# Kernel tuning notes

Measured on AMD Instinct MI355X. Metric: run time of the kernel, lower is better.

Reference implementation:

```python
import jax, jax.numpy as jnp
import numpy as np

B, A, N = 4, 256, 64
NCB, NF, NSB, DIMS = 128, 128, 50, 3
CUTOFF = 5.0
LOG2 = 0.6931471805599453


def ssp(x):
    # shifted softplus: softplus(x) - ln(2)
    return jax.nn.softplus(x) - LOG2


def mlp2(x, W1, b1, W2, b2):
    # Dense(act=ssp) -> Dense(linear)
    return ssp(x @ W1 + b1) @ W2 + b2


def setup_inputs():
    key = jax.random.key(0)
    ks = jax.random.split(key, 32)

    def w(k, shape):
        return jax.random.normal(k, shape, jnp.float32) / np.sqrt(shape[0]).astype(np.float32)

    return {
        "xi": jax.random.normal(ks[0], (B, A, NCB), jnp.float32),
        "r_ij": jax.random.uniform(ks[1], (B, A, N), jnp.float32) * CUTOFF,
        "cos_ij": jax.random.normal(ks[2], (B, A, N, DIMS), jnp.float32),
        "f_ij": jax.random.normal(ks[3], (B, A, N, NSB), jnp.float32),
        "neighbor_mask": jnp.ones((B, A, N), jnp.float32),
        "filt_W1": w(ks[4], (NSB, NF)), "filt_b1": jnp.zeros((NF,), jnp.float32),
        "filt_W2": w(ks[5], (NF, NF)), "filt_b2": jnp.zeros((NF,), jnp.float32),
        "in2f_W": w(ks[6], (NCB, NF)),
        "f2out_W": w(ks[7], (NF, NF)), "f2out_b": jnp.zeros((NF,), jnp.float32),
        "atom_W1": w(ks[8], (NF, NF)), "atom_b1": jnp.zeros((NF,), jnp.float32),
        "atom_W2": w(ks[9], (NF, NCB)), "atom_b2": jnp.zeros((NCB,), jnp.float32),
        "pair_W1": w(ks[10], (NF, NF)), "pair_b1": jnp.zeros((NF,), jnp.float32),
        "pair_W2": w(ks[11], (NF, NCB)), "pair_b2": jnp.zeros((NCB,), jnp.float32),
        "env_W1": w(ks[12], (NF, NF)), "env_b1": jnp.zeros((NF,), jnp.float32),
        "env_W2": w(ks[13], (NF, NCB)), "env_b2": jnp.zeros((NCB,), jnp.float32),
        "neighbors": jax.random.randint(ks[14], (B, A, N), 0, A),
    }


def reference(xi, r_ij, cos_ij, f_ij, neighbor_mask,
              filt_W1, filt_b1, filt_W2, filt_b2, in2f_W, f2out_W, f2out_b,
              atom_W1, atom_b1, atom_W2, atom_b2,
              pair_W1, pair_b1, pair_W2, pair_b2,
              env_W1, env_b1, env_W2, env_b2, neighbors):
    bidx = jnp.arange(B)[:, None, None]
    # --- FTLayer: filter net on Gaussian-expanded distances, cosine cutoff ---
    Wf = ssp(f_ij @ filt_W1 + filt_b1) @ filt_W2 + filt_b2            # [B,A,N,NF]
    C = 0.5 * (jnp.cos(r_ij * (jnp.pi / CUTOFF)) + 1.0) * (r_ij < CUTOFF)
    Wf = Wf * C[..., None]
    yj = (xi @ in2f_W)[bidx, neighbors]                               # gather -> [B,A,N,NF]
    v = ssp((yj * Wf) @ f2out_W + f2out_b)                            # [B,A,N,NF]
    # --- atom-wise channel (masked neighbor sum) ---
    vi = jnp.sum(v * neighbor_mask[..., None], axis=2)                # [B,A,NF]
    vi = mlp2(vi, atom_W1, atom_b1, atom_W2, atom_b2)                 # [B,A,NCB]
    # --- pair tensor: outer product with cosine basis ---
    vij = mlp2(v, pair_W1, pair_b1, pair_W2, pair_b2)                 # [B,A,N,NCB]
    Vij = vij[..., None] * cos_ij[..., None, :]                       # [B,A,N,NCB,3]
    # --- environment tensor: masked agg then second-order neighbor gather ---
    vik = mlp2(v, env_W1, env_b1, env_W2, env_b2)                     # [B,A,N,NCB]
    Vik = jnp.sum(vik[..., None] * cos_ij[..., None, :]
                  * neighbor_mask[..., None, None], axis=2)           # [B,A,NCB,3]
    Vjl = Vik[bidx, neighbors]                                        # [B,A,N,NCB,3]
    V = Vij + Vik[:, :, None] + Vjl                                   # [B,A,N,NCB,3]
    return vi, V
```

## Files before the change

kernel.cpp:

```cpp
#include <hip/hip_runtime.h>
#include <hip/hip_bf16.h>
#include <math.h>

#define B 4
#define A 256
#define NN 64
#define NCB 128
#define NF 128
#define NSB 50
#define BA (B*A)
#define PAIRS (BA*NN)

typedef __bf16 bf;
typedef __attribute__((ext_vector_type(8))) __bf16 bfrag8;
typedef __attribute__((ext_vector_type(4))) float ffrag4;

__device__ __attribute__((aligned(16))) bf    g_yib[BA*NF];
__device__ __attribute__((aligned(16))) bf    g_vij[(size_t)PAIRS*NCB];
__device__ __attribute__((aligned(16))) float g_vik[BA*NCB*3];
__device__ __attribute__((aligned(16))) bf g_tf1[NF*64];
__device__ __attribute__((aligned(16))) bf g_tf2[NF*NF];
__device__ __attribute__((aligned(16))) bf g_tfo[NF*NF];
__device__ __attribute__((aligned(16))) bf g_tp1[NF*NF];
__device__ __attribute__((aligned(16))) bf g_tp2[NF*NF];
__device__ __attribute__((aligned(16))) bf g_te1[NF*NF];
__device__ __attribute__((aligned(16))) bf g_te2[NF*NF];

__device__ __forceinline__ float ssp(float x){
    float e = __expf(-fabsf(x));
    return fmaxf(x, 0.f) + __logf(1.f + e) - 0.6931471805599453f;
}

__global__ __launch_bounds__(256)
void k_wt(const float* __restrict__ f1, const float* __restrict__ f2,
          const float* __restrict__ fo, const float* __restrict__ p1,
          const float* __restrict__ p2, const float* __restrict__ e1,
          const float* __restrict__ e2){
    int s = blockIdx.x >> 3, part = blockIdx.x & 7;
    const float* src; bf* dst; int kb, realK;
    if (s == 0){ src = f1; dst = g_tf1; kb = 6; realK = NSB; }
    else {
        kb = 7; realK = 128;
        src = (s==1)?f2:(s==2)?fo:(s==3)?p1:(s==4)?p2:(s==5)?e1:e2;
        dst = (s==1)?g_tf2:(s==2)?g_tfo:(s==3)?g_tp1:(s==4)?g_tp2:(s==5)?g_te1:g_te2;
    }
    int total = NF << kb;
    int chunk = total >> 3;
    int end = (part + 1) * chunk;
    for (int e = part*chunk + threadIdx.x; e < end; e += 256){
        int n = e >> kb, k = e & ((1<<kb)-1);
        dst[e] = (k < realK) ? (bf)src[k*NF + n] : (bf)0.f;
    }
}

__global__ __launch_bounds__(NF)
void k_yi(const float* __restrict__ xi, const float* __restrict__ W){
    int row = blockIdx.x, f = threadIdx.x;
    __shared__ float x[NCB];
    x[f] = xi[row*NCB + f];
    __syncthreads();
    float s = 0.f;
    #pragma unroll 16
    for (int c = 0; c < NCB; c++) s += x[c]*W[c*NF + f];
    g_yib[row*NF + f] = (bf)s;
}

__device__ __forceinline__ void stage_w128(bf* __restrict__ sW, const bf* __restrict__ g,
                                           int half, int tid){
    #pragma unroll
    for (int i = 0; i < 4; i++){
        int r  = i*16 + (tid >> 4);
        int cp = (tid & 15)*8;
        *(bfrag8*)&sW[r*136 + cp] = *(const bfrag8*)&g[(half*64 + r)*128 + cp];
    }
}
__device__ __forceinline__ void stage_w64(bf* __restrict__ sW, const bf* __restrict__ g,
                                          int half, int tid){
    #pragma unroll
    for (int i = 0; i < 2; i++){
        int r  = i*32 + (tid >> 3);
        int cp = (tid & 7)*8;
        *(bfrag8*)&sW[r*72 + cp] = *(const bfrag8*)&g[(half*64 + r)*64 + cp];
    }
}
__device__ __forceinline__ void gemm4(const bf* __restrict__ sW, const bfrag8 afr[4],
                                      ffrag4 acc[4], int q, int c16){
    #pragma unroll
    for (int nt = 0; nt < 4; nt++){
        ffrag4 a = {0.f,0.f,0.f,0.f};
        #pragma unroll
        for (int kt = 0; kt < 4; kt++){
            bfrag8 bv = *(const bfrag8*)&sW[(nt*16 + c16)*136 + kt*32 + q*8];
            a = __builtin_amdgcn_mfma_f32_16x16x32_bf16(afr[kt], bv, a, 0, 0, 0);
        }
        acc[nt] = a;
    }
}
__device__ __forceinline__ void gemm2(const bf* __restrict__ sW, const bfrag8 afr[2],
                                      ffrag4 acc[4], int q, int c16){
    #pragma unroll
    for (int nt = 0; nt < 4; nt++){
        ffrag4 a = {0.f,0.f,0.f,0.f};
        #pragma unroll
        for (int kt = 0; kt < 2; kt++){
            bfrag8 bv = *(const bfrag8*)&sW[(nt*16 + c16)*72 + kt*32 + q*8];
            a = __builtin_amdgcn_mfma_f32_16x16x32_bf16(afr[kt], bv, a, 0, 0, 0);
        }
        acc[nt] = a;
    }
}

#define RDA4(DST) { _Pragma("unroll") for (int kt = 0; kt < 4; kt++) \
    DST[kt] = *(const bfrag8*)&sX[arow*136 + kt*32 + q*8]; }

#define EPI_SSP(BIASP, H) \
    { _Pragma("unroll") for (int nt = 0; nt < 4; nt++){ \
        int col = ((H)*4 + nt)*16 + c16; \
        float bias = BIASP[col]; \
        _Pragma("unroll") for (int rg = 0; rg < 4; rg++){ \
            int row = w*16 + q*4 + rg; \
            sX[row*136 + col] = (bf)ssp(acc[nt][rg] + bias); \
        } } }

#define EPI_LIN(BIASP, H) \
    { _Pragma("unroll") for (int nt = 0; nt < 4; nt++){ \
        int col = ((H)*4 + nt)*16 + c16; \
        float bias = BIASP[col]; \
        _Pragma("unroll") for (int rg = 0; rg < 4; rg++){ \
            int row = w*16 + q*4 + rg; \
            sX[row*136 + col] = (bf)(acc[nt][rg] + bias); \
        } } }

__global__ __launch_bounds__(256, 4)
void k_main(const float* __restrict__ r_ij, const float* __restrict__ cos_ij,
            const float* __restrict__ f_ij, const float* __restrict__ mask,
            const int* __restrict__ neighbors,
            const float* __restrict__ fb1, const float* __restrict__ fb2,
            const float* __restrict__ f2b,
            const float* __restrict__ aW1, const float* __restrict__ ab1,
            const float* __restrict__ aW2, const float* __restrict__ ab2,
            const float* __restrict__ pb1, const float* __restrict__ pb2,
            const float* __restrict__ eb1, const float* __restrict__ eb2,
            float* __restrict__ out_vi){
    const int tid  = threadIdx.x;
    const int ba   = blockIdx.x;
    const int b    = ba >> 8;
    const int w    = tid >> 6;
    const int lane = tid & 63;
    const int q    = lane >> 4;
    const int c16  = lane & 15;
    const int arow = w*16 + c16;

    __shared__ __attribute__((aligned(16))) bf sW[64*136];
    __shared__ __attribute__((aligned(16))) bf sX[64*136];
    __shared__ float sCosM[64*4];
    __shared__ float sCr[64];
    __shared__ int   sJb[64];

    #pragma unroll
    for (int i = 0; i < 16; i++){
        int row = w*16 + i;
        float v = (lane < NSB) ? f_ij[(ba*64 + row)*NSB + lane] : 0.f;
        sX[row*136 + lane] = (bf)v;
    }
    if (lane < 16){
        int row = w*16 + lane;
        int p = ba*64 + row;
        sCosM[row*4+0] = cos_ij[p*3+0];
        sCosM[row*4+1] = cos_ij[p*3+1];
        sCosM[row*4+2] = cos_ij[p*3+2];
        sCosM[row*4+3] = mask[p];
        float r = r_ij[p];
        sCr[row] = (r < 5.f) ? 0.5f*(__cosf(r*0.62831853071795864769f) + 1.f) : 0.f;
        int j = neighbors[p] & (A-1);
        sJb[row] = (b*A + j)*NF;
    }

    bfrag8 afr[4], afrV[4], afr2[2]; ffrag4 acc[4];

    #pragma unroll
    for (int kt = 0; kt < 2; kt++) afr2[kt] = *(const bfrag8*)&sX[arow*136 + kt*32 + q*8];
    #pragma unroll
    for (int half = 0; half < 2; half++){
        if (half) __syncthreads();
        stage_w64(sW, g_tf1, half, tid);
        __syncthreads();
        gemm2(sW, afr2, acc, q, c16);
        EPI_SSP(fb1, half);
    }
    RDA4(afr);
    __syncthreads();

    #pragma unroll
    for (int half = 0; half < 2; half++){
        if (half) __syncthreads();
        stage_w128(sW, g_tf2, half, tid);
        __syncthreads();
        gemm4(sW, afr, acc, q, c16);
        #pragma unroll
        for (int nt = 0; nt < 4; nt++){
            int col = (half*4 + nt)*16 + c16;
            float bias = fb2[col];
            #pragma unroll
            for (int rg = 0; rg < 4; rg++){
                int row = w*16 + q*4 + rg;
                float wf = (acc[nt][rg] + bias) * sCr[row];
                sX[row*136 + col] = (bf)((float)g_yib[sJb[row] + col] * wf);
            }
        }
    }
    RDA4(afr);
    __syncthreads();

    float vsAll[8];
    #pragma unroll
    for (int t = 0; t < 8; t++) vsAll[t] = 0.f;
    #pragma unroll
    for (int half = 0; half < 2; half++){
        if (half) __syncthreads();
        stage_w128(sW, g_tfo, half, tid);
        __syncthreads();
        gemm4(sW, afr, acc, q, c16);
        #pragma unroll
        for (int nt = 0; nt < 4; nt++){
            int col = (half*4 + nt)*16 + c16;
            float bias = f2b[col];
            #pragma unroll
            for (int rg = 0; rg < 4; rg++){
                int row = w*16 + q*4 + rg;
                float v = ssp(acc[nt][rg] + bias);
                sX[row*136 + col] = (bf)v;
                vsAll[half*4 + nt] += v * sCosM[row*4+3];
            }
        }
    }
    RDA4(afrV);
    __syncthreads();

    #pragma unroll
    for (int half = 0; half < 2; half++){
        if (half) __syncthreads();
        stage_w128(sW, g_tp1, half, tid);
        __syncthreads();
        gemm4(sW, afrV, acc, q, c16);
        EPI_SSP(pb1, half);
    }
    RDA4(afr);
    __syncthreads();

    #pragma unroll
    for (int half = 0; half < 2; half++){
        if (half) __syncthreads();
        stage_w128(sW, g_tp2, half, tid);
        __syncthreads();
        gemm4(sW, afr, acc, q, c16);
        EPI_LIN(pb2, half);
    }
    #pragma unroll
    for (int i = 0; i < 4; i++){
        int row = w*16 + i*4 + (lane >> 4);
        int cp  = c16*8;
        *(bfrag8*)&g_vij[((size_t)ba*64 + row)*128 + cp] = *(const bfrag8*)&sX[row*136 + cp];
    }
    __syncthreads();

    #pragma unroll
    for (int half = 0; half < 2; half++){
        if (half) __syncthreads();
        stage_w128(sW, g_te1, half, tid);
        __syncthreads();
        gemm4(sW, afrV, acc, q, c16);
        EPI_SSP(eb1, half);
    }
    RDA4(afr);
    __syncthreads();

    float vkAll[8][3];
    #pragma unroll
    for (int t = 0; t < 8; t++){ vkAll[t][0]=0.f; vkAll[t][1]=0.f; vkAll[t][2]=0.f; }
    #pragma unroll
    for (int half = 0; half < 2; half++){
        if (half) __syncthreads();
        stage_w128(sW, g_te2, half, tid);
        __syncthreads();
        gemm4(sW, afr, acc, q, c16);
        #pragma unroll
        for (int nt = 0; nt < 4; nt++){
            float bias = eb2[(half*4 + nt)*16 + c16];
            #pragma unroll
            for (int rg = 0; rg < 4; rg++){
                int row = w*16 + q*4 + rg;
                float vik = (acc[nt][rg] + bias) * sCosM[row*4+3];
                vkAll[half*4 + nt][0] += vik * sCosM[row*4+0];
                vkAll[half*4 + nt][1] += vik * sCosM[row*4+1];
                vkAll[half*4 + nt][2] += vik * sCosM[row*4+2];
            }
        }
    }

    __syncthreads();
    float* const sVs   = (float*)sX;
    float* const sVk   = (float*)((char*)sX + 2048);
    float* const sVsum = (float*)((char*)sX + 8192);
    float* const sHa   = (float*)((char*)sX + 8704);
    #pragma unroll
    for (int t = 0; t < 8; t++){
        float v = vsAll[t];
        v += __shfl_xor(v, 16);
        v += __shfl_xor(v, 32);
        if (q == 0) sVs[w*128 + t*16 + c16] = v;
    }
    #pragma unroll
    for (int t = 0; t < 8; t++){
        #pragma unroll
        for (int d = 0; d < 3; d++){
            float v = vkAll[t][d];
            v += __shfl_xor(v, 16);
            v += __shfl_xor(v, 32);
            if (q == 0) sVk[w*384 + (t*16 + c16)*3 + d] = v;
        }
    }
    __syncthreads();

    for (int e = tid; e < 384; e += 256)
        g_vik[ba*384 + e] = sVk[e] + sVk[384+e] + sVk[768+e] + sVk[1152+e];
    if (tid < 128)
        sVsum[tid] = sVs[tid] + sVs[128+tid] + sVs[256+tid] + sVs[384+tid];
    __syncthreads();
    if (tid < 128){
        float acc2 = ab1[tid];
        #pragma unroll 16
        for (int k = 0; k < 128; k++) acc2 += sVsum[k]*aW1[k*128 + tid];
        sHa[tid] = ssp(acc2);
    }
    __syncthreads();
    if (tid < 128){
        float acc2 = ab2[tid];
        #pragma unroll 16
        for (int k = 0; k < 128; k++) acc2 += sHa[k]*aW2[k*128 + tid];
        out_vi[ba*128 + tid] = acc2;
    }
}

__global__ __launch_bounds__(256)
void k_V(const float* __restrict__ cos_ij, const int* __restrict__ nbrs,
         float* __restrict__ outV){
    const int ba  = blockIdx.x;
    const int b   = ba >> 8;
    const int tid = threadIdx.x;
    __shared__ __attribute__((aligned(16))) bf sVij[64*128];
    __shared__ float sVa[384];
    __shared__ float sC[64*4];
    __shared__ int   sJ[64];
    #pragma unroll
    for (int i = 0; i < 4; i++){
        int e8 = tid + i*256;
        *(bfrag8*)&sVij[e8*8] = *(const bfrag8*)&g_vij[(size_t)ba*8192 + e8*8];
    }
    for (int e = tid; e < 384; e += 256) sVa[e] = g_vik[ba*384 + e];
    if (tid < 64){
        int p = ba*64 + tid;
        sJ[tid] = (b*A + (nbrs[p] & (A-1)))*384;
        sC[tid*4+0] = cos_ij[p*3+0];
        sC[tid*4+1] = cos_ij[p*3+1];
        sC[tid*4+2] = cos_ij[p*3+2];
    }
    __syncthreads();
    float* const oBase = outV + (size_t)ba*24576;
    #pragma unroll 4
    for (int it = 0; it < 24; it++){
        int idx = (it*256 + tid)*4;
        int pl  = idx / 384;
        int e0  = idx - pl*384;
        ffrag4 va = *(const ffrag4*)&sVa[e0];
        ffrag4 vj = *(const ffrag4*)(g_vik + sJ[pl] + e0);
        ffrag4 o;
        #pragma unroll
        for (int j2 = 0; j2 < 4; j2++){
            int e = e0 + j2;
            int c = e / 3;
            int d = e - c*3;
            float vv = (float)sVij[pl*128 + c];
            o[j2] = fmaf(vv, sC[pl*4+d], va[j2] + vj[j2]);
        }
        __builtin_nontemporal_store(o, (ffrag4*)(oBase + idx));
    }
}

extern "C" void kernel_launch(void* const* d_in, const int* in_sizes, int n_in,
                              void* d_out, int out_size, void* d_ws, size_t ws_size,
                              hipStream_t stream){
    const float* xi      = (const float*)d_in[0];
    const float* r_ij    = (const float*)d_in[1];
    const float* cos_ij  = (const float*)d_in[2];
    const float* f_ij    = (const float*)d_in[3];
    const float* nmask   = (const float*)d_in[4];
    const float* fW1     = (const float*)d_in[5];
    const float* fb1     = (const float*)d_in[6];
    const float* fW2     = (const float*)d_in[7];
    const float* fb2     = (const float*)d_in[8];
    const float* in2f_W  = (const float*)d_in[9];
    const float* f2W     = (const float*)d_in[10];
    const float* f2b     = (const float*)d_in[11];
    const float* aW1     = (const float*)d_in[12];
    const float* ab1     = (const float*)d_in[13];
    const float* aW2     = (const float*)d_in[14];
    const float* ab2     = (const float*)d_in[15];
    const float* pW1     = (const float*)d_in[16];
    const float* pb1     = (const float*)d_in[17];
    const float* pW2     = (const float*)d_in[18];
    const float* pb2     = (const float*)d_in[19];
    const float* eW1     = (const float*)d_in[20];
    const float* eb1     = (const float*)d_in[21];
    const float* eW2     = (const float*)d_in[22];
    const float* eb2     = (const float*)d_in[23];
    const int*  nbrs     = (const int*)d_in[24];

    float* out_vi = (float*)d_out;
    float* outV   = (float*)d_out + BA*NCB;

    k_wt<<<56, 256, 0, stream>>>(fW1, fW2, f2W, pW1, pW2, eW1, eW2);
    k_yi<<<BA, NF, 0, stream>>>(xi, in2f_W);

    k_main<<<BA, 256, 0, stream>>>(r_ij, cos_ij, f_ij, nmask, nbrs,
                                   fb1, fb2, f2b,
                                   aW1, ab1, aW2, ab2,
                                   pb1, pb2, eb1, eb2,
                                   out_vi);

    k_V<<<BA, 256, 0, stream>>>(cos_ij, nbrs, outV);
}
```

Before: 235.8 us.

## Fuse V assembly into main kernel via grid barrier, merge prep kernels

Merges the weight-transpose and yi projection kernels into one launch, and folds the k_V output kernel into the main kernel. Pair-MLP outputs stay in registers instead of round-tripping through a bf16 global buffer, and a software grid-wide atomic barrier waits until all g_vik entries are written before the neighbor gather. The cost is a spin barrier that needs all 1024 blocks co-resident, which risks deadlock if occupancy is lower than expected. The output stores are also now scalar, strided writes rather than 16-byte vectorised ones.

```diff
diff --git a/kernel.cpp b/kernel.cpp
--- a/kernel.cpp
+++ b/kernel.cpp
@@ -16,8 +16,8 @@
 typedef __attribute__((ext_vector_type(4))) float ffrag4;
 
 __device__ __attribute__((aligned(16))) bf    g_yib[BA*NF];
-__device__ __attribute__((aligned(16))) bf    g_vij[(size_t)PAIRS*NCB];
 __device__ __attribute__((aligned(16))) float g_vik[BA*NCB*3];
+__device__ int g_bar = 0;
 __device__ __attribute__((aligned(16))) bf g_tf1[NF*64];
 __device__ __attribute__((aligned(16))) bf g_tf2[NF*NF];
 __device__ __attribute__((aligned(16))) bf g_tfo[NF*NF];
@@ -32,37 +32,41 @@
 }
 
 __global__ __launch_bounds__(256)
-void k_wt(const float* __restrict__ f1, const float* __restrict__ f2,
-          const float* __restrict__ fo, const float* __restrict__ p1,
-          const float* __restrict__ p2, const float* __restrict__ e1,
-          const float* __restrict__ e2){
-    int s = blockIdx.x >> 3, part = blockIdx.x & 7;
-    const float* src; bf* dst; int kb, realK;
-    if (s == 0){ src = f1; dst = g_tf1; kb = 6; realK = NSB; }
-    else {
-        kb = 7; realK = 128;
-        src = (s==1)?f2:(s==2)?fo:(s==3)?p1:(s==4)?p2:(s==5)?e1:e2;
-        dst = (s==1)?g_tf2:(s==2)?g_tfo:(s==3)?g_tp1:(s==4)?g_tp2:(s==5)?g_te1:g_te2;
-    }
-    int total = NF << kb;
-    int chunk = total >> 3;
-    int end = (part + 1) * chunk;
-    for (int e = part*chunk + threadIdx.x; e < end; e += 256){
-        int n = e >> kb, k = e & ((1<<kb)-1);
-        dst[e] = (k < realK) ? (bf)src[k*NF + n] : (bf)0.f;
-    }
-}
-
-__global__ __launch_bounds__(NF)
-void k_yi(const float* __restrict__ xi, const float* __restrict__ W){
-    int row = blockIdx.x, f = threadIdx.x;
-    __shared__ float x[NCB];
-    x[f] = xi[row*NCB + f];
-    __syncthreads();
-    float s = 0.f;
-    #pragma unroll 16
-    for (int c = 0; c < NCB; c++) s += x[c]*W[c*NF + f];
-    g_yib[row*NF + f] = (bf)s;
+void k_pre(const float* __restrict__ f1, const float* __restrict__ f2,
+           const float* __restrict__ fo, const float* __restrict__ p1,
+           const float* __restrict__ p2, const float* __restrict__ e1,
+           const float* __restrict__ e2,
+           const float* __restrict__ xi, const float* __restrict__ W){
+    __shared__ float x[2][NCB];
+    int blk = blockIdx.x;
+    if (blk == 0 && threadIdx.x == 0)
+        __hip_atomic_store(&g_bar, 0, __ATOMIC_RELAXED, __HIP_MEMORY_SCOPE_AGENT);
+    if (blk < 56){
+        int s = blk >> 3, part = blk & 7;
+        const float* src; bf* dst; int kb, realK;
+        if (s == 0){ src = f1; dst = g_tf1; kb = 6; realK = NSB; }
+        else {
+            kb = 7; realK = 128;
+            src = (s==1)?f2:(s==2)?fo:(s==3)?p1:(s==4)?p2:(s==5)?e1:e2;
+            dst = (s==1)?g_tf2:(s==2)?g_tfo:(s==3)?g_tp1:(s==4)?g_tp2:(s==5)?g_te1:g_te2;
+        }
+        int total = NF << kb;
+        int chunk = total >> 3;
+        int end = (part + 1) * chunk;
+        for (int e = part*chunk + threadIdx.x; e < end; e += 256){
+            int n = e >> kb, k = e & ((1<<kb)-1);
+            dst[e] = (k < realK) ? (bf)src[k*NF + n] : (bf)0.f;
+        }
+    } else {
+        int r = threadIdx.x >> 7, f = threadIdx.x & 127;
+        int row = (blk - 56)*2 + r;
+        x[r][f] = xi[row*NCB + f];
+        __syncthreads();
+        float s = 0.f;
+        #pragma unroll 16
+        for (int c = 0; c < NCB; c++) s += x[r][c]*W[c*NF + f];
+        g_yib[row*NF + f] = (bf)s;
+    }
 }
 
 __device__ __forceinline__ void stage_w128(bf* __restrict__ sW, const bf* __restrict__ g,
@@ -122,26 +126,17 @@
             sX[row*136 + col] = (bf)ssp(acc[nt][rg] + bias); \
         } } }
 
-#define EPI_LIN(BIASP, H) \
-    { _Pragma("unroll") for (int nt = 0; nt < 4; nt++){ \
-        int col = ((H)*4 + nt)*16 + c16; \
-        float bias = BIASP[col]; \
-        _Pragma("unroll") for (int rg = 0; rg < 4; rg++){ \
-            int row = w*16 + q*4 + rg; \
-            sX[row*136 + col] = (bf)(acc[nt][rg] + bias); \
-        } } }
-
 __global__ __launch_bounds__(256, 4)
-void k_main(const float* __restrict__ r_ij, const float* __restrict__ cos_ij,
-            const float* __restrict__ f_ij, const float* __restrict__ mask,
-            const int* __restrict__ neighbors,
-            const float* __restrict__ fb1, const float* __restrict__ fb2,
-            const float* __restrict__ f2b,
-            const float* __restrict__ aW1, const float* __restrict__ ab1,
-            const float* __restrict__ aW2, const float* __restrict__ ab2,
-            const float* __restrict__ pb1, const float* __restrict__ pb2,
-            const float* __restrict__ eb1, const float* __restrict__ eb2,
-            float* __restrict__ out_vi){
+void k_fused(const float* __restrict__ r_ij, const float* __restrict__ cos_ij,
+             const float* __restrict__ f_ij, const float* __restrict__ mask,
+             const int* __restrict__ neighbors,
+             const float* __restrict__ fb1, const float* __restrict__ fb2,
+             const float* __restrict__ f2b,
+             const float* __restrict__ aW1, const float* __restrict__ ab1,
+             const float* __restrict__ aW2, const float* __restrict__ ab2,
+             const float* __restrict__ pb1, const float* __restrict__ pb2,
+             const float* __restrict__ eb1, const float* __restrict__ eb2,
+             float* __restrict__ out_vi, float* __restrict__ outV){
     const int tid  = threadIdx.x;
     const int ba   = blockIdx.x;
     const int b    = ba >> 8;
@@ -248,19 +243,20 @@
     RDA4(afr);
     __syncthreads();
 
+    float vijR[8][4];
     #pragma unroll
     for (int half = 0; half < 2; half++){
         if (half) __syncthreads();
         stage_w128(sW, g_tp2, half, tid);
         __syncthreads();
         gemm4(sW, afr, acc, q, c16);
-        EPI_LIN(pb2, half);
-    }
-    #pragma unroll
-    for (int i = 0; i < 4; i++){
-        int row = w*16 + i*4 + (lane >> 4);
-        int cp  = c16*8;
-        *(bfrag8*)&g_vij[((size_t)ba*64 + row)*128 + cp] = *(const bfrag8*)&sX[row*136 + cp];
+        #pragma unroll
+        for (int nt = 0; nt < 4; nt++){
+            float bias = pb2[(half*4 + nt)*16 + c16];
+            #pragma unroll
+            for (int rg = 0; rg < 4; rg++)
+                vijR[half*4 + nt][rg] = acc[nt][rg] + bias;
+        }
     }
     __syncthreads();
 
@@ -303,6 +299,7 @@
     float* const sVk   = (float*)((char*)sX + 2048);
     float* const sVsum = (float*)((char*)sX + 8192);
     float* const sHa   = (float*)((char*)sX + 8704);
+    float* const sVa   = (float*)((char*)sX + 12288);
     #pragma unroll
     for (int t = 0; t < 8; t++){
         float v = vsAll[t];
@@ -322,8 +319,11 @@
     }
     __syncthreads();
 
-    for (int e = tid; e < 384; e += 256)
-        g_vik[ba*384 + e] = sVk[e] + sVk[384+e] + sVk[768+e] + sVk[1152+e];
+    for (int e = tid; e < 384; e += 256){
+        float s = sVk[e] + sVk[384+e] + sVk[768+e] + sVk[1152+e];
+        g_vik[ba*384 + e] = s;
+        sVa[e] = s;
+    }
     if (tid < 128)
         sVsum[tid] = sVs[tid] + sVs[128+tid] + sVs[256+tid] + sVs[384+tid];
     __syncthreads();
@@ -340,50 +340,32 @@
         for (int k = 0; k < 128; k++) acc2 += sHa[k]*aW2[k*128 + tid];
         out_vi[ba*128 + tid] = acc2;
     }
-}
-
-__global__ __launch_bounds__(256)
-void k_V(const float* __restrict__ cos_ij, const int* __restrict__ nbrs,
-         float* __restrict__ outV){
-    const int ba  = blockIdx.x;
-    const int b   = ba >> 8;
-    const int tid = threadIdx.x;
-    __shared__ __attribute__((aligned(16))) bf sVij[64*128];
-    __shared__ float sVa[384];
-    __shared__ float sC[64*4];
-    __shared__ int   sJ[64];
-    #pragma unroll
-    for (int i = 0; i < 4; i++){
-        int e8 = tid + i*256;
-        *(bfrag8*)&sVij[e8*8] = *(const bfrag8*)&g_vij[(size_t)ba*8192 + e8*8];
-    }
-    for (int e = tid; e < 384; e += 256) sVa[e] = g_vik[ba*384 + e];
-    if (tid < 64){
-        int p = ba*64 + tid;
-        sJ[tid] = (b*A + (nbrs[p] & (A-1)))*384;
-        sC[tid*4+0] = cos_ij[p*3+0];
-        sC[tid*4+1] = cos_ij[p*3+1];
-        sC[tid*4+2] = cos_ij[p*3+2];
-    }
-    __syncthreads();
-    float* const oBase = outV + (size_t)ba*24576;
-    #pragma unroll 4
-    for (int it = 0; it < 24; it++){
-        int idx = (it*256 + tid)*4;
-        int pl  = idx / 384;
-        int e0  = idx - pl*384;
-        ffrag4 va = *(const ffrag4*)&sVa[e0];
-        ffrag4 vj = *(const ffrag4*)(g_vik + sJ[pl] + e0);
-        ffrag4 o;
-        #pragma unroll
-        for (int j2 = 0; j2 < 4; j2++){
-            int e = e0 + j2;
-            int c = e / 3;
-            int d = e - c*3;
-            float vv = (float)sVij[pl*128 + c];
-            o[j2] = fmaf(vv, sC[pl*4+d], va[j2] + vj[j2]);
-        }
-        __builtin_nontemporal_store(o, (ffrag4*)(oBase + idx));
+
+    __threadfence();
+    __syncthreads();
+    if (tid == 0){
+        __hip_atomic_fetch_add(&g_bar, 1, __ATOMIC_ACQ_REL, __HIP_MEMORY_SCOPE_AGENT);
+        while (__hip_atomic_load(&g_bar, __ATOMIC_ACQUIRE, __HIP_MEMORY_SCOPE_AGENT) < BA)
+            __builtin_amdgcn_s_sleep(8);
+    }
+    __syncthreads();
+
+    float* const oV = outV + (size_t)ba*24576;
+    #pragma unroll
+    for (int t = 0; t < 8; t++){
+        int col = t*16 + c16;
+        float a0 = sVa[col*3+0], a1 = sVa[col*3+1], a2 = sVa[col*3+2];
+        #pragma unroll
+        for (int rg = 0; rg < 4; rg++){
+            int row = w*16 + q*4 + rg;
+            float vv = vijR[t][rg];
+            const float* vj = g_vik + sJb[row]*3 + col*3;
+            float c0 = sCosM[row*4+0], c1 = sCosM[row*4+1], c2 = sCosM[row*4+2];
+            float* o = oV + row*384 + col*3;
+            __builtin_nontemporal_store(fmaf(vv, c0, a0 + vj[0]), o+0);
+            __builtin_nontemporal_store(fmaf(vv, c1, a1 + vj[1]), o+1);
+            __builtin_nontemporal_store(fmaf(vv, c2, a2 + vj[2]), o+2);
+        }
     }
 }
 
@@ -419,14 +401,11 @@
     float* out_vi = (float*)d_out;
     float* outV   = (float*)d_out + BA*NCB;
 
-    k_wt<<<56, 256, 0, stream>>>(fW1, fW2, f2W, pW1, pW2, eW1, eW2);
-    k_yi<<<BA, NF, 0, stream>>>(xi, in2f_W);
-
-    k_main<<<BA, 256, 0, stream>>>(r_ij, cos_ij, f_ij, nmask, nbrs,
-                                   fb1, fb2, f2b,
-                                   aW1, ab1, aW2, ab2,
-                                   pb1, pb2, eb1, eb2,
-                                   out_vi);
-
-    k_V<<<BA, 256, 0, stream>>>(cos_ij, nbrs, outV);
-}
+    k_pre<<<568, 256, 0, stream>>>(fW1, fW2, f2W, pW1, pW2, eW1, eW2, xi, in2f_W);
+
+    k_fused<<<BA, 256, 0, stream>>>(r_ij, cos_ij, f_ij, nmask, nbrs,
+                                    fb1, fb2, f2b,
+                                    aW1, ab1, aW2, ab2,
+                                    pb1, pb2, eb1, eb2,
+                                    out_vi, outV);
+}
```

Result: slower. 470.7 us (+99.6%).

## Process two atoms per block and double-buffer weight staging in k_main

Applied to the files above, without the earlier changes.

k_main now runs 512 threads per block covering two atoms (128 pair rows), so each staged weight tile is reused by twice as many rows. Weight halves are double-buffered in shared memory, and the next half or next layer's weights load while the current half's MFMA and epilogue run, which removes one barrier per stage. The costs are more shared memory per block (about 70KB), fewer blocks in the grid (512), and a launch bound of 512 threads with 4 blocks that puts heavy pressure on registers.

```diff
diff --git a/kernel.cpp b/kernel.cpp
--- a/kernel.cpp
+++ b/kernel.cpp
@@ -68,20 +68,17 @@
 __device__ __forceinline__ void stage_w128(bf* __restrict__ sW, const bf* __restrict__ g,
                                            int half, int tid){
     #pragma unroll
-    for (int i = 0; i < 4; i++){
-        int r  = i*16 + (tid >> 4);
+    for (int i = 0; i < 2; i++){
+        int r  = i*32 + (tid >> 4);
         int cp = (tid & 15)*8;
         *(bfrag8*)&sW[r*136 + cp] = *(const bfrag8*)&g[(half*64 + r)*128 + cp];
     }
 }
 __device__ __forceinline__ void stage_w64(bf* __restrict__ sW, const bf* __restrict__ g,
                                           int half, int tid){
-    #pragma unroll
-    for (int i = 0; i < 2; i++){
-        int r  = i*32 + (tid >> 3);
-        int cp = (tid & 7)*8;
-        *(bfrag8*)&sW[r*72 + cp] = *(const bfrag8*)&g[(half*64 + r)*64 + cp];
-    }
+    int r  = tid >> 3;
+    int cp = (tid & 7)*8;
+    *(bfrag8*)&sW[r*72 + cp] = *(const bfrag8*)&g[(half*64 + r)*64 + cp];
 }
 __device__ __forceinline__ void gemm4(const bf* __restrict__ sW, const bfrag8 afr[4],
                                       ffrag4 acc[4], int q, int c16){
@@ -131,7 +128,39 @@
             sX[row*136 + col] = (bf)(acc[nt][rg] + bias); \
         } } }
 
-__global__ __launch_bounds__(256, 4)
+#define EPI_S2(H) \
+    { _Pragma("unroll") for (int nt = 0; nt < 4; nt++){ \
+        int col = ((H)*4 + nt)*16 + c16; \
+        float bias = fb2[col]; \
+        _Pragma("unroll") for (int rg = 0; rg < 4; rg++){ \
+            int row = w*16 + q*4 + rg; \
+            float wf = (acc[nt][rg] + bias) * sCr[row]; \
+            sX[row*136 + col] = (bf)((float)g_yib[sJb[row] + col] * wf); \
+        } } }
+
+#define EPI_S3(H) \
+    { _Pragma("unroll") for (int nt = 0; nt < 4; nt++){ \
+        int col = ((H)*4 + nt)*16 + c16; \
+        float bias = f2b[col]; \
+        _Pragma("unroll") for (int rg = 0; rg < 4; rg++){ \
+            int row = w*16 + q*4 + rg; \
+            float v = ssp(acc[nt][rg] + bias); \
+            sX[row*136 + col] = (bf)v; \
+            vsAll[(H)*4 + nt] += v * sCosM[row*4+3]; \
+        } } }
+
+#define EPI_VIK(H) \
+    { _Pragma("unroll") for (int nt = 0; nt < 4; nt++){ \
+        float bias = eb2[((H)*4 + nt)*16 + c16]; \
+        _Pragma("unroll") for (int rg = 0; rg < 4; rg++){ \
+            int row = w*16 + q*4 + rg; \
+            float vik = (acc[nt][rg] + bias) * sCosM[row*4+3]; \
+            vkAll[(H)*4 + nt][0] += vik * sCosM[row*4+0]; \
+            vkAll[(H)*4 + nt][1] += vik * sCosM[row*4+1]; \
+            vkAll[(H)*4 + nt][2] += vik * sCosM[row*4+2]; \
+        } } }
+
+__global__ __launch_bounds__(512, 4)
 void k_main(const float* __restrict__ r_ij, const float* __restrict__ cos_ij,
             const float* __restrict__ f_ij, const float* __restrict__ mask,
             const int* __restrict__ neighbors,
@@ -143,29 +172,30 @@
             const float* __restrict__ eb1, const float* __restrict__ eb2,
             float* __restrict__ out_vi){
     const int tid  = threadIdx.x;
-    const int ba   = blockIdx.x;
-    const int b    = ba >> 8;
+    const int blk  = blockIdx.x;
     const int w    = tid >> 6;
     const int lane = tid & 63;
     const int q    = lane >> 4;
     const int c16  = lane & 15;
     const int arow = w*16 + c16;
 
-    __shared__ __attribute__((aligned(16))) bf sW[64*136];
-    __shared__ __attribute__((aligned(16))) bf sX[64*136];
-    __shared__ float sCosM[64*4];
-    __shared__ float sCr[64];
-    __shared__ int   sJb[64];
+    __shared__ __attribute__((aligned(16))) bf sWp[2][64*136];
+    __shared__ __attribute__((aligned(16))) bf sX[128*136];
+    __shared__ float sCosM[128*4];
+    __shared__ float sCr[128];
+    __shared__ int   sJb[128];
 
     #pragma unroll
     for (int i = 0; i < 16; i++){
         int row = w*16 + i;
-        float v = (lane < NSB) ? f_ij[(ba*64 + row)*NSB + lane] : 0.f;
+        float v = (lane < NSB) ? f_ij[((size_t)blk*128 + row)*NSB + lane] : 0.f;
         sX[row*136 + lane] = (bf)v;
     }
     if (lane < 16){
         int row = w*16 + lane;
-        int p = ba*64 + row;
+        int p = blk*128 + row;
+        int ba = blk*2 + (row >> 6);
+        int b  = ba >> 8;
         sCosM[row*4+0] = cos_ij[p*3+0];
         sCosM[row*4+1] = cos_ij[p*3+1];
         sCosM[row*4+2] = cos_ij[p*3+2];
@@ -177,132 +207,90 @@
     }
 
     bfrag8 afr[4], afrV[4], afr2[2]; ffrag4 acc[4];
+    float vsAll[8];
+    #pragma unroll
+    for (int t = 0; t < 8; t++) vsAll[t] = 0.f;
+    float vkAll[8][3];
+    #pragma unroll
+    for (int t = 0; t < 8; t++){ vkAll[t][0]=0.f; vkAll[t][1]=0.f; vkAll[t][2]=0.f; }
 
     #pragma unroll
     for (int kt = 0; kt < 2; kt++) afr2[kt] = *(const bfrag8*)&sX[arow*136 + kt*32 + q*8];
-    #pragma unroll
-    for (int half = 0; half < 2; half++){
-        if (half) __syncthreads();
-        stage_w64(sW, g_tf1, half, tid);
-        __syncthreads();
-        gemm2(sW, afr2, acc, q, c16);
-        EPI_SSP(fb1, half);
-    }
+
+    stage_w64(sWp[0], g_tf1, 0, tid);
+    __syncthreads();
+
+    stage_w64(sWp[1], g_tf1, 1, tid);
+    gemm2(sWp[0], afr2, acc, q, c16);
+    EPI_SSP(fb1, 0);
+    __syncthreads();
+    stage_w128(sWp[0], g_tf2, 0, tid);
+    gemm2(sWp[1], afr2, acc, q, c16);
+    EPI_SSP(fb1, 1);
     RDA4(afr);
     __syncthreads();
-
-    #pragma unroll
-    for (int half = 0; half < 2; half++){
-        if (half) __syncthreads();
-        stage_w128(sW, g_tf2, half, tid);
-        __syncthreads();
-        gemm4(sW, afr, acc, q, c16);
-        #pragma unroll
-        for (int nt = 0; nt < 4; nt++){
-            int col = (half*4 + nt)*16 + c16;
-            float bias = fb2[col];
-            #pragma unroll
-            for (int rg = 0; rg < 4; rg++){
-                int row = w*16 + q*4 + rg;
-                float wf = (acc[nt][rg] + bias) * sCr[row];
-                sX[row*136 + col] = (bf)((float)g_yib[sJb[row] + col] * wf);
-            }
-        }
-    }
+    stage_w128(sWp[1], g_tf2, 1, tid);
+    gemm4(sWp[0], afr, acc, q, c16);
+    EPI_S2(0);
+    __syncthreads();
+    stage_w128(sWp[0], g_tfo, 0, tid);
+    gemm4(sWp[1], afr, acc, q, c16);
+    EPI_S2(1);
     RDA4(afr);
     __syncthreads();
-
-    float vsAll[8];
-    #pragma unroll
-    for (int t = 0; t < 8; t++) vsAll[t] = 0.f;
-    #pragma unroll
-    for (int half = 0; half < 2; half++){
-        if (half) __syncthreads();
-        stage_w128(sW, g_tfo, half, tid);
-        __syncthreads();
-        gemm4(sW, afr, acc, q, c16);
-        #pragma unroll
-        for (int nt = 0; nt < 4; nt++){
-            int col = (half*4 + nt)*16 + c16;
-            float bias = f2b[col];
-            #pragma unroll
-            for (int rg = 0; rg < 4; rg++){
-                int row = w*16 + q*4 + rg;
-                float v = ssp(acc[nt][rg] + bias);
-                sX[row*136 + col] = (bf)v;
-                vsAll[half*4 + nt] += v * sCosM[row*4+3];
-            }
-        }
-    }
+    stage_w128(sWp[1], g_tfo, 1, tid);
+    gemm4(sWp[0], afr, acc, q, c16);
+    EPI_S3(0);
+    __syncthreads();
+    stage_w128(sWp[0], g_tp1, 0, tid);
+    gemm4(sWp[1], afr, acc, q, c16);
+    EPI_S3(1);
     RDA4(afrV);
     __syncthreads();
-
-    #pragma unroll
-    for (int half = 0; half < 2; half++){
-        if (half) __syncthreads();
-        stage_w128(sW, g_tp1, half, tid);
-        __syncthreads();
-        gemm4(sW, afrV, acc, q, c16);
-        EPI_SSP(pb1, half);
-    }
+    stage_w128(sWp[1], g_tp1, 1, tid);
+    gemm4(sWp[0], afrV, acc, q, c16);
+    EPI_SSP(pb1, 0);
+    __syncthreads();
+    stage_w128(sWp[0], g_tp2, 0, tid);
+    gemm4(sWp[1], afrV, acc, q, c16);
+    EPI_SSP(pb1, 1);
     RDA4(afr);
     __syncthreads();
-
-    #pragma unroll
-    for (int half = 0; half < 2; half++){
-        if (half) __syncthreads();
-        stage_w128(sW, g_tp2, half, tid);
-        __syncthreads();
-        gemm4(sW, afr, acc, q, c16);
-        EPI_LIN(pb2, half);
-    }
+    stage_w128(sWp[1], g_tp2, 1, tid);
+    gemm4(sWp[0], afr, acc, q, c16);
+    EPI_LIN(pb2, 0);
+    __syncthreads();
+    stage_w128(sWp[0], g_te1, 0, tid);
+    gemm4(sWp[1], afr, acc, q, c16);
+    EPI_LIN(pb2, 1);
     #pragma unroll
     for (int i = 0; i < 4; i++){
         int row = w*16 + i*4 + (lane >> 4);
         int cp  = c16*8;
-        *(bfrag8*)&g_vij[((size_t)ba*64 + row)*128 + cp] = *(const bfrag8*)&sX[row*136 + cp];
-    }
-    __syncthreads();
-
-    #pragma unroll
-    for (int half = 0; half < 2; half++){
-        if (half) __syncthreads();
-        stage_w128(sW, g_te1, half, tid);
-        __syncthreads();
-        gemm4(sW, afrV, acc, q, c16);
-        EPI_SSP(eb1, half);
-    }
+        *(bfrag8*)&g_vij[((size_t)blk*128 + row)*128 + cp] = *(const bfrag8*)&sX[row*136 + cp];
+    }
+    __syncthreads();
+    stage_w128(sWp[1], g_te1, 1, tid);
+    gemm4(sWp[0], afrV, acc, q, c16);
+    EPI_SSP(eb1, 0);
+    __syncthreads();
+    stage_w128(sWp[0], g_te2, 0, tid);
+    gemm4(sWp[1], afrV, acc, q, c16);
+    EPI_SSP(eb1, 1);
     RDA4(afr);
     __syncthreads();
-
-    float vkAll[8][3];
-    #pragma unroll
-    for (int t = 0; t < 8; t++){ vkAll[t][0]=0.f; vkAll[t][1]=0.f; vkAll[t][2]=0.f; }
-    #pragma unroll
-    for (int half = 0; half < 2; half++){
-        if (half) __syncthreads();
-        stage_w128(sW, g_te2, half, tid);
-        __syncthreads();
-        gemm4(sW, afr, acc, q, c16);
-        #pragma unroll
-        for (int nt = 0; nt < 4; nt++){
-            float bias = eb2[(half*4 + nt)*16 + c16];
-            #pragma unroll
-            for (int rg = 0; rg < 4; rg++){
-                int row = w*16 + q*4 + rg;
-                float vik = (acc[nt][rg] + bias) * sCosM[row*4+3];
-                vkAll[half*4 + nt][0] += vik * sCosM[row*4+0];
-                vkAll[half*4 + nt][1] += vik * sCosM[row*4+1];
-                vkAll[half*4 + nt][2] += vik * sCosM[row*4+2];
-            }
-        }
-    }
+    stage_w128(sWp[1], g_te2, 1, tid);
+    gemm4(sWp[0], afr, acc, q, c16);
+    EPI_VIK(0);
+    __syncthreads();
+    gemm4(sWp[1], afr, acc, q, c16);
+    EPI_VIK(1);
 
     __syncthreads();
     float* const sVs   = (float*)sX;
-    float* const sVk   = (float*)((char*)sX + 2048);
-    float* const sVsum = (float*)((char*)sX + 8192);
-    float* const sHa   = (float*)((char*)sX + 8704);
+    float* const sVk   = (float*)((char*)sX + 4096);
+    float* const sVsum = (float*)((char*)sX + 16384);
+    float* const sHa   = (float*)((char*)sX + 17408);
     #pragma unroll
     for (int t = 0; t < 8; t++){
         float v = vsAll[t];
@@ -322,23 +310,31 @@
     }
     __syncthreads();
 
-    for (int e = tid; e < 384; e += 256)
-        g_vik[ba*384 + e] = sVk[e] + sVk[384+e] + sVk[768+e] + sVk[1152+e];
-    if (tid < 128)
-        sVsum[tid] = sVs[tid] + sVs[128+tid] + sVs[256+tid] + sVs[384+tid];
-    __syncthreads();
-    if (tid < 128){
-        float acc2 = ab1[tid];
+    for (int e = tid; e < 768; e += 512){
+        int at = e / 384, em = e - at*384;
+        const float* p0 = sVk + (at*4)*384;
+        g_vik[(blk*2 + at)*384 + em] = p0[em] + p0[384+em] + p0[768+em] + p0[1152+em];
+    }
+    if (tid < 256){
+        int at = tid >> 7, f = tid & 127;
+        const float* p0 = sVs + (at*4)*128;
+        sVsum[tid] = p0[f] + p0[128+f] + p0[256+f] + p0[384+f];
+    }
+    __syncthreads();
+    if (tid < 256){
+        int at = tid >> 7, f = tid & 127;
+        float acc2 = ab1[f];
         #pragma unroll 16
-        for (int k = 0; k < 128; k++) acc2 += sVsum[k]*aW1[k*128 + tid];
+        for (int k = 0; k < 128; k++) acc2 += sVsum[at*128+k]*aW1[k*128 + f];
         sHa[tid] = ssp(acc2);
     }
     __syncthreads();
-    if (tid < 128){
-        float acc2 = ab2[tid];
+    if (tid < 256){
+        int at = tid >> 7, f = tid & 127;
+        float acc2 = ab2[f];
         #pragma unroll 16
-        for (int k = 0; k < 128; k++) acc2 += sHa[k]*aW2[k*128 + tid];
-        out_vi[ba*128 + tid] = acc2;
+        for (int k = 0; k < 128; k++) acc2 += sHa[at*128+k]*aW2[k*128 + f];
+        out_vi[(blk*2 + at)*128 + f] = acc2;
     }
 }
 
@@ -422,11 +418,11 @@
     k_wt<<<56, 256, 0, stream>>>(fW1, fW2, f2W, pW1, pW2, eW1, eW2);
     k_yi<<<BA, NF, 0, stream>>>(xi, in2f_W);
 
-    k_main<<<BA, 256, 0, stream>>>(r_ij, cos_ij, f_ij, nmask, nbrs,
-                                   fb1, fb2, f2b,
-                                   aW1, ab1, aW2, ab2,
-                                   pb1, pb2, eb1, eb2,
-                                   out_vi);
+    k_main<<<BA/2, 512, 0, stream>>>(r_ij, cos_ij, f_ij, nmask, nbrs,
+                                     fb1, fb2, f2b,
+                                     aW1, ab1, aW2, ab2,
+                                     pb1, pb2, eb1, eb2,
+                                     out_vi);
 
     k_V<<<BA, 256, 0, stream>>>(cos_ij, nbrs, outV);
 }
```

New measurement: 240.8 us. 2.1% more time.

## Stage weights via direct global-to-LDS loads with XOR-swizzled layout

Applied to the files above, without the earlier changes.

Weight tiles are now copied into shared memory with global_load_lds, which moves data from global memory straight into LDS without passing through registers. The unpadded LDS layout uses an XOR swizzle to avoid bank conflicts, and that swizzle is applied once in the weight-transpose kernel. The GEMM B-fragment reads use the matching XOR index. This is meant to cut register pressure and VGPR round-trips when staging weights, but it depends on the swizzle staying consistent between the prep kernel and the readers, and on waits being placed correctly.

```diff
diff --git a/kernel.cpp b/kernel.cpp
--- a/kernel.cpp
+++ b/kernel.cpp
@@ -31,25 +31,36 @@
     return fmaxf(x, 0.f) + __logf(1.f + e) - 0.6931471805599453f;
 }
 
+__device__ __forceinline__ void gload_lds16(const void* g, void* l){
+    __builtin_amdgcn_global_load_lds(
+        (const __attribute__((address_space(1))) void*)g,
+        (__attribute__((address_space(3))) void*)l, 16, 0, 0);
+}
+
 __global__ __launch_bounds__(256)
 void k_wt(const float* __restrict__ f1, const float* __restrict__ f2,
           const float* __restrict__ fo, const float* __restrict__ p1,
           const float* __restrict__ p2, const float* __restrict__ e1,
           const float* __restrict__ e2){
     int s = blockIdx.x >> 3, part = blockIdx.x & 7;
-    const float* src; bf* dst; int kb, realK;
-    if (s == 0){ src = f1; dst = g_tf1; kb = 6; realK = NSB; }
-    else {
-        kb = 7; realK = 128;
-        src = (s==1)?f2:(s==2)?fo:(s==3)?p1:(s==4)?p2:(s==5)?e1:e2;
-        dst = (s==1)?g_tf2:(s==2)?g_tfo:(s==3)?g_tp1:(s==4)?g_tp2:(s==5)?g_te1:g_te2;
-    }
-    int total = NF << kb;
-    int chunk = total >> 3;
-    int end = (part + 1) * chunk;
-    for (int e = part*chunk + threadIdx.x; e < end; e += 256){
-        int n = e >> kb, k = e & ((1<<kb)-1);
-        dst[e] = (k < realK) ? (bf)src[k*NF + n] : (bf)0.f;
+    if (s == 0){
+        int base = part*1024;
+        for (int e = base + threadIdx.x; e < base + 1024; e += 256){
+            int n = e >> 6, kl = e & 63;
+            int c = kl >> 3, j = kl & 7;
+            int ok = ((c ^ (n & 7)) << 3) + j;
+            g_tf1[e] = (ok < NSB) ? (bf)f1[ok*NF + n] : (bf)0.f;
+        }
+    } else {
+        const float* src = (s==1)?f2:(s==2)?fo:(s==3)?p1:(s==4)?p2:(s==5)?e1:e2;
+        bf* dst = (s==1)?g_tf2:(s==2)?g_tfo:(s==3)?g_tp1:(s==4)?g_tp2:(s==5)?g_te1:g_te2;
+        int base = part*2048;
+        for (int e = base + threadIdx.x; e < base + 2048; e += 256){
+            int n = e >> 7, kl = e & 127;
+            int c = kl >> 3, j = kl & 7;
+            int ok = ((c ^ (n & 15)) << 3) + j;
+            dst[e] = (bf)src[ok*NF + n];
+        }
     }
 }
 
@@ -67,30 +78,34 @@
 
 __device__ __forceinline__ void stage_w128(bf* __restrict__ sW, const bf* __restrict__ g,
                                            int half, int tid){
+    int wv = tid >> 6, lane = tid & 63;
+    const bf* gs = g + (size_t)half*8192;
     #pragma unroll
     for (int i = 0; i < 4; i++){
-        int r  = i*16 + (tid >> 4);
-        int cp = (tid & 15)*8;
-        *(bfrag8*)&sW[r*136 + cp] = *(const bfrag8*)&g[(half*64 + r)*128 + cp];
+        int cb = wv*256 + i*64;
+        gload_lds16(gs + (size_t)(cb + lane)*8, &sW[cb*8]);
     }
 }
 __device__ __forceinline__ void stage_w64(bf* __restrict__ sW, const bf* __restrict__ g,
                                           int half, int tid){
+    int wv = tid >> 6, lane = tid & 63;
+    const bf* gs = g + (size_t)half*4096;
     #pragma unroll
     for (int i = 0; i < 2; i++){
-        int r  = i*32 + (tid >> 3);
-        int cp = (tid & 7)*8;
-        *(bfrag8*)&sW[r*72 + cp] = *(const bfrag8*)&g[(half*64 + r)*64 + cp];
+        int cb = wv*128 + i*64;
+        gload_lds16(gs + (size_t)(cb + lane)*8, &sW[cb*8]);
     }
 }
 __device__ __forceinline__ void gemm4(const bf* __restrict__ sW, const bfrag8 afr[4],
                                       ffrag4 acc[4], int q, int c16){
     #pragma unroll
     for (int nt = 0; nt < 4; nt++){
+        int n = nt*16 + c16;
         ffrag4 a = {0.f,0.f,0.f,0.f};
         #pragma unroll
         for (int kt = 0; kt < 4; kt++){
-            bfrag8 bv = *(const bfrag8*)&sW[(nt*16 + c16)*136 + kt*32 + q*8];
+            int ch = (kt*4 + q) ^ c16;
+            bfrag8 bv = *(const bfrag8*)&sW[n*128 + ch*8];
             a = __builtin_amdgcn_mfma_f32_16x16x32_bf16(afr[kt], bv, a, 0, 0, 0);
         }
         acc[nt] = a;
@@ -100,10 +115,12 @@
                                       ffrag4 acc[4], int q, int c16){
     #pragma unroll
     for (int nt = 0; nt < 4; nt++){
+        int n = nt*16 + c16;
         ffrag4 a = {0.f,0.f,0.f,0.f};
         #pragma unroll
         for (int kt = 0; kt < 2; kt++){
-            bfrag8 bv = *(const bfrag8*)&sW[(nt*16 + c16)*72 + kt*32 + q*8];
+            int ch = (kt*4 + q) ^ (c16 & 7);
+            bfrag8 bv = *(const bfrag8*)&sW[n*64 + ch*8];
             a = __builtin_amdgcn_mfma_f32_16x16x32_bf16(afr[kt], bv, a, 0, 0, 0);
         }
         acc[nt] = a;
@@ -151,7 +168,7 @@
     const int c16  = lane & 15;
     const int arow = w*16 + c16;
 
-    __shared__ __attribute__((aligned(16))) bf sW[64*136];
+    __shared__ __attribute__((aligned(16))) bf sW[8192];
     __shared__ __attribute__((aligned(16))) bf sX[64*136];
     __shared__ float sCosM[64*4];
     __shared__ float sCr[64];
@@ -160,7 +177,7 @@
     #pragma unroll
     for (int i = 0; i < 16; i++){
         int row = w*16 + i;
-        float v = (lane < NSB) ? f_ij[(ba*64 + row)*NSB + lane] : 0.f;
+        float v = (lane < NSB) ? f_ij[((size_t)ba*64 + row)*NSB + lane] : 0.f;
         sX[row*136 + lane] = (bf)v;
     }
     if (lane < 16){
```

After: 238.7 us. No clear change (+1.2%).
